# Performance work log

Hardware: AMD Instinct MI355X
Metric: run time of the kernel (lower is better)

## Reference

```python
import jax, jax.numpy as jnp
import numpy as np

B, S, D, O = 16, 1024, 512, 512
THRESH = 0.9
NEG_SLOPE = 0.2  # PyG GATConv default leaky_relu slope


def setup_inputs() -> dict:
    key = jax.random.key(0)
    kx, kw, kas, kad, kb = jax.random.split(key, 5)
    # uniform in [0.2, 1) so cosine similarities straddle the 0.9 threshold
    x = jax.random.uniform(kx, (B, S, D), dtype=jnp.float32, minval=0.2, maxval=1.0)
    scale = 1.0 / np.sqrt(D)
    W = jax.random.normal(kw, (D, O), dtype=jnp.float32) * scale       # GATConv lin weight
    att_src = jax.random.normal(kas, (O,), dtype=jnp.float32) * scale  # att_src [1,1,O] squeezed
    att_dst = jax.random.normal(kad, (O,), dtype=jnp.float32) * scale  # att_dst [1,1,O] squeezed
    bias = jnp.zeros((O,), dtype=jnp.float32)
    return {"distilled_features": x, "W": W, "att_src": att_src, "att_dst": att_dst, "bias": bias}


def reference(distilled_features, W, att_src, att_dst, bias):
    x = distilled_features  # [B, S, D]
    s = x.shape[1]
    # --- edge construction: cosine similarity > 0.9, i < j, edge i->j (src->dst) ---
    norm = jnp.sqrt(jnp.sum(x * x, axis=-1, keepdims=True))
    normed = x / jnp.maximum(norm, 1e-12)  # F.normalize eps
    sim = jnp.einsum('bsd,btd->bst', normed, normed)  # [B, S, S], symmetric
    # adj[b, dst, src] = True if edge src->dst exists
    src_lt_dst = jnp.tril(jnp.ones((s, s), dtype=bool), k=-1)  # [dst, src] with src < dst
    eye = jnp.eye(s, dtype=bool)                                # self-loops (PyG default)
    adj = ((sim > THRESH) & src_lt_dst[None]) | eye[None]       # [B, dst, src]
    # --- GATConv, heads=1 (dropout inactive at inference) ---
    h = jnp.einsum('bsd,do->bso', x, W)            # [B, S, O]
    a_src = jnp.einsum('bso,o->bs', h, att_src)    # per-source logit
    a_dst = jnp.einsum('bso,o->bs', h, att_dst)    # per-dest logit
    e = jax.nn.leaky_relu(a_dst[:, :, None] + a_src[:, None, :], negative_slope=NEG_SLOPE)
    e = jnp.where(adj, e, -jnp.inf)
    attn = jax.nn.softmax(e, axis=-1)              # softmax over sources per dest
    out = jnp.einsum('bts,bso->bto', attn, h) + bias
    return jax.nn.relu(out)
```

## Files before the change

### kernel.cpp

```cpp
#include <hip/hip_runtime.h>
#include <hip/hip_bf16.h>
#include <stdint.h>

#define NB 16
#define NS 1024
#define ND 512
#define NO 512
#define NROW (NB*NS)
#define SIM_BAND 1.5e-3f
#define LIST_CAP 524288

typedef float f32x4 __attribute__((ext_vector_type(4)));
typedef _Float16 f16x8 __attribute__((ext_vector_type(8)));

__global__ __launch_bounds__(256) void k_prep_w2(const float* __restrict__ W,
                                                 const float* __restrict__ att_src,
                                                 const float* __restrict__ att_dst,
                                                 _Float16* __restrict__ Wf,
                                                 float* __restrict__ watt_s,
                                                 float* __restrict__ watt_d) {
  __shared__ float as_[512], ad_[512];
  int blk = blockIdx.x, tid = threadIdx.x;
  if (blk < 32) {
    int mt = blk>>3, k0c = blk&7;
    size_t base = ((size_t)(mt*8 + k0c))*8192;
    #pragma unroll
    for (int pp = 0; pp < 4; ++pp) {
      int id = pp*256 + tid;
      int kb = id>>9, m = (id>>6)&7, g = (id>>4)&3, r = id&15;
      int o = mt*128 + m*16 + r;
      int d0 = k0c*64 + kb*32 + g*8;
      union { _Float16 h[8]; uint4 u; } pk;
      #pragma unroll
      for (int j = 0; j < 8; ++j) pk.h[j] = (_Float16)W[(size_t)(d0+j)*NO + o];
      *(uint4*)&Wf[base + id*8] = pk.u;
    }
  } else {
    as_[tid] = att_src[tid]; as_[tid+256] = att_src[tid+256];
    ad_[tid] = att_dst[tid]; ad_[tid+256] = att_dst[tid+256];
    __syncthreads();
    int d = (blk-32)*256 + tid;
    const float* wr = W + (size_t)d*NO;
    float s = 0.f, dd = 0.f;
    for (int o = 0; o < NO; o += 4) {
      float4 w = *(const float4*)&wr[o];
      s  = fmaf(w.x, as_[o], fmaf(w.y, as_[o+1], fmaf(w.z, as_[o+2], fmaf(w.w, as_[o+3], s))));
      dd = fmaf(w.x, ad_[o], fmaf(w.y, ad_[o+1], fmaf(w.z, ad_[o+2], fmaf(w.w, ad_[o+3], dd))));
    }
    watt_s[d] = s;
    watt_d[d] = dd;
  }
}

__global__ __launch_bounds__(256) void k_prep_y(const float* __restrict__ x,
                                                _Float16* __restrict__ yf,
                                                float* __restrict__ rnorm,
                                                float* __restrict__ a_src,
                                                float* __restrict__ a_dst,
                                                const float* __restrict__ watt_s,
                                                const float* __restrict__ watt_d,
                                                int* __restrict__ counter) {
  __shared__ float ws_[512], wd_[512];
  int tid = threadIdx.x, blk = blockIdx.x;
  if (blk == 0 && tid == 0) *counter = 0;
  ws_[tid] = watt_s[tid]; ws_[tid+256] = watt_s[tid+256];
  wd_[tid] = watt_d[tid]; wd_[tid+256] = watt_d[tid+256];
  __syncthreads();
  int r = tid>>2, q = tid&3;
  int grow = blk*64 + r;
  const float* xr = x + (size_t)grow*ND + q*128;
  float ssq = 0.f, as = 0.f, ad = 0.f;
  #pragma unroll
  for (int c8 = 0; c8 < 16; ++c8) {
    float4 v0 = *(const float4*)&xr[c8*8];
    float4 v1 = *(const float4*)&xr[c8*8+4];
    float vv[8] = {v0.x,v0.y,v0.z,v0.w,v1.x,v1.y,v1.z,v1.w};
    #pragma unroll
    for (int j = 0; j < 8; ++j) {
      int c = q*128 + c8*8 + j;
      ssq = fmaf(vv[j], vv[j], ssq);
      as  = fmaf(vv[j], ws_[c], as);
      ad  = fmaf(vv[j], wd_[c], ad);
    }
  }
  ssq += __shfl_xor(ssq, 1, 64); ssq += __shfl_xor(ssq, 2, 64);
  as  += __shfl_xor(as, 1, 64);  as  += __shfl_xor(as, 2, 64);
  ad  += __shfl_xor(ad, 1, 64);  ad  += __shfl_xor(ad, 2, 64);
  float rn = 1.0f / fmaxf(sqrtf(ssq), 1e-12f);
  if (q == 0) { rnorm[grow] = rn; a_src[grow] = as; a_dst[grow] = ad; }
  int trow = grow & (NS-1), b = grow >> 10;
  int m = (trow>>4)&7, rr = trow&15;
  size_t tilebase = ((size_t)(b*8 + (trow>>7)))*65536;
  #pragma unroll
  for (int c8 = 0; c8 < 16; ++c8) {
    int col = q*128 + c8*8;
    int k0c = col>>6, cc = col&63, kb = cc>>5, g = (cc>>3)&3;
    int id = kb*512 + m*64 + g*16 + rr;
    size_t off = tilebase + (size_t)k0c*8192 + id*8;
    float4 v0 = *(const float4*)&xr[c8*8];
    float4 v1 = *(const float4*)&xr[c8*8+4];
    float vv[8] = {v0.x,v0.y,v0.z,v0.w,v1.x,v1.y,v1.z,v1.w};
    union { _Float16 h[8]; uint4 u; } pk;
    #pragma unroll
    for (int j = 0; j < 8; ++j) pk.h[j] = (_Float16)(vv[j]*rn);
    *(uint4*)&yf[off] = pk.u;
  }
}

#define FRAG_LD(AH, BH, APTR, BPTR, h) do { \
    _Pragma("unroll") \
    for (int q_ = 0; q_ < 4; ++q_) { \
      AH[q_] = *(const f16x8*)&APTR[Abase + (size_t)(h)*4096 + (size_t)(aq + q_)*512]; \
      BH[q_] = *(const f16x8*)&BPTR[Bbase + (size_t)(h)*4096 + (size_t)(bq + q_)*512]; \
    } \
  } while(0)

#define MFMA16(AH, BH) do { \
    _Pragma("unroll") \
    for (int mi_ = 0; mi_ < 4; ++mi_) \
      _Pragma("unroll") \
      for (int ni_ = 0; ni_ < 4; ++ni_) \
        acc[mi_][ni_] = __builtin_amdgcn_mfma_f32_16x16x32_f16(AH[mi_], BH[ni_], acc[mi_][ni_], 0,0,0); \
  } while(0)

__global__ __launch_bounds__(256) void k_sim_ht(const _Float16* __restrict__ yf,
                                                const _Float16* __restrict__ Wf,
                                                const float* __restrict__ rnorm,
                                                uint16_t* __restrict__ Mbits,
                                                unsigned int* __restrict__ list,
                                                int* __restrict__ counter,
                                                _Float16* __restrict__ htf) {
  __shared__ __align__(16) _Float16 sbuf[16384];
  int bid0 = blockIdx.x;
  int tid = threadIdx.x, wid = tid>>6, lane = tid&63;
  int wm = (wid>>1)*64, wn = (wid&1)*64;
  int aq = (wm>>4), bq = (wn>>4);
  if (bid0 < 576) {
    int swz = (bid0 & 7)*72 + (bid0 >> 3);
    int b = swz / 36, p = swz - b*36;
    int ti = 0;
    while ((ti+1)*(ti+2)/2 <= p) ++ti;
    int tj = p - ti*(ti+1)/2;
    size_t Abase = ((size_t)(b*8+ti))*65536 + (size_t)lane*8;
    size_t Bbase = ((size_t)(b*8+tj))*65536 + (size_t)lane*8;
    f32x4 acc[4][4] = {};
    f16x8 A0[4], B0[4], A1[4], B1[4];
    FRAG_LD(A0, B0, yf, yf, 0);
    for (int hp = 0; hp < 8; ++hp) {
      FRAG_LD(A1, B1, yf, yf, 2*hp+1);
      MFMA16(A0, B0);
      if (hp < 7) FRAG_LD(A0, B0, yf, yf, 2*hp+2);
      MFMA16(A1, B1);
    }
    int hi = lane>>4, colL = lane&15;
    #pragma unroll
    for (int mi = 0; mi < 4; ++mi) {
      #pragma unroll
      for (int r2 = 0; r2 < 4; ++r2) {
        int t_g = ti*128 + wm + mi*16 + hi*4 + r2;
        int git = b*NS + t_g;
        #pragma unroll
        for (int ni = 0; ni < 4; ++ni) {
          int s_g = tj*128 + wn + ni*16 + colL;
          float sim = acc[mi][ni][r2];
          bool bit = (s_g == t_g) || (s_g < t_g && sim > 0.9f);
          bool cond = (s_g < t_g) && (fabsf(sim - 0.9f) <= SIM_BAND);
          unsigned long long bb = __ballot(cond);
          if (bb) {
            int leader = __ffsll((unsigned long long)bb) - 1;
            int base = 0;
            if (lane == leader) base = atomicAdd(counter, __popcll(bb));
            base = __shfl(base, leader, 64);
            if (cond) {
              int idx = base + __popcll(bb & ((1ULL<<lane)-1ULL));
              if (idx < LIST_CAP) list[idx] = ((unsigned)b<<20) | ((unsigned)t_g<<10) | (unsigned)s_g;
            }
          }
          unsigned long long bal = __ballot(bit);
          if (colL == 0) {
            uint16_t slice = (uint16_t)((bal >> (hi*16)) & 0xFFFFull);
            Mbits[(size_t)git*64 + ((tj*128 + wn + ni*16)>>4)] = slice;
          }
        }
      }
    }
  } else {
    int bidh = bid0 - 576;
    int swz = (bidh&7)*64 + (bidh>>3);
    int mt = swz&3, it = swz>>2;
    int b = it>>3, tblk = it&7;
    size_t Abase = ((size_t)mt)*65536 + (size_t)lane*8;
    size_t Bbase = ((size_t)(b*8+tblk))*65536 + (size_t)lane*8;
    f32x4 acc[4][4] = {};
    f16x8 A0[4], B0[4], A1[4], B1[4];
    FRAG_LD(A0, B0, Wf, yf, 0);
    for (int hp = 0; hp < 8; ++hp) {
      FRAG_LD(A1, B1, Wf, yf, 2*hp+1);
      MFMA16(A0, B0);
      if (hp < 7) FRAG_LD(A0, B0, Wf, yf, 2*hp+2);
      MFMA16(A1, B1);
    }
    {
      int rbase = (lane>>4)*4, colL = lane&15;
      #pragma unroll
      for (int ni = 0; ni < 4; ++ni) {
        int i_local = wn + ni*16 + colL;
        int gn = it*128 + i_local;
        float xn = 1.0f / rnorm[gn];
        int tsel = i_local>>6, ic = i_local&63;
        int kb = ic>>5, g = (ic>>3)&3, j = ic&7;
        int base = tsel*8192 + (kb*512 + g*16)*8 + j;
        #pragma unroll
        for (int mi = 0; mi < 4; ++mi)
          #pragma unroll
          for (int r2 = 0; r2 < 4; ++r2) {
            int o_local = wm + mi*16 + rbase + r2;
            int m = o_local>>4, r = o_local&15;
            sbuf[base + (m*64 + r)*8] = (_Float16)(acc[mi][ni][r2] * xn);
          }
      }
    }
    __syncthreads();
    {
      size_t gbase = ((size_t)((mt*NB + b)*16 + tblk*2))*8192;
      const uint4* src = (const uint4*)sbuf;
      uint4* dst = (uint4*)(htf + gbase);
      #pragma unroll
      for (int k = 0; k < 8; ++k) dst[tid + k*256] = src[tid + k*256];
    }
  }
}

__global__ __launch_bounds__(256) void k_recheck(const float* __restrict__ x,
                                                 const float* __restrict__ rnorm,
                                                 uint32_t* __restrict__ Mw,
                                                 const unsigned int* __restrict__ list,
                                                 const int* __restrict__ counter) {
  int n = *counter;
  if (n > LIST_CAP) n = LIST_CAP;
  int lane = threadIdx.x & 63;
  int gwave = blockIdx.x*4 + (threadIdx.x>>6);
  for (int p = gwave; p < n; p += 8192) {
    unsigned v = list[p];
    int b = v>>20, t = (v>>10)&1023, s = v&1023;
    const float* xt = x + ((size_t)(b*NS + t))*ND + lane*8;
    const float* xs = x + ((size_t)(b*NS + s))*ND + lane*8;
    float4 t0 = *(const float4*)xt;
    float4 t1 = *(const float4*)(xt+4);
    float4 s0 = *(const float4*)xs;
    float4 s1 = *(const float4*)(xs+4);
    float d = 0.f;
    d = fmaf(t0.x,s0.x, fmaf(t0.y,s0.y, fmaf(t0.z,s0.z, fmaf(t0.w,s0.w, d))));
    d = fmaf(t1.x,s1.x, fmaf(t1.y,s1.y, fmaf(t1.z,s1.z, fmaf(t1.w,s1.w, d))));
    #pragma unroll
    for (int off = 32; off > 0; off >>= 1) d += __shfl_xor(d, off, 64);
    if (lane == 0) {
      float sim = d * rnorm[b*NS+t] * rnorm[b*NS+s];
      int git = b*NS + t;
      uint32_t bmask = 1u << (s&31);
      if (sim > 0.9f) atomicOr (&Mw[(size_t)git*32 + (s>>5)], bmask);
      else            atomicAnd(&Mw[(size_t)git*32 + (s>>5)], ~bmask);
    }
  }
}

__global__ __launch_bounds__(256) void k_softmax(const uint32_t* __restrict__ Mw,
                                                 const float* __restrict__ a_src,
                                                 const float* __restrict__ a_dst,
                                                 _Float16* __restrict__ Pf) {
  __shared__ __align__(16) _Float16 pbuf[4][1032];
  int wid = threadIdx.x>>6, lane = threadIdx.x&63;
  int rowid = blockIdx.x*4 + wid;
  int t = rowid & (NS-1), b = rowid >> 10;
  int n = t + 1;
  const float* as = a_src + b*NS;
  float adv = a_dst[rowid];
  uint32_t w = Mw[(size_t)rowid*32 + (lane>>1)];
  uint32_t bits16 = (lane&1) ? (w>>16) : (w & 0xFFFFu);
  int s0 = lane*16;
  float4 a0 = *(const float4*)&as[s0];
  float4 a1 = *(const float4*)&as[s0+4];
  float4 a2 = *(const float4*)&as[s0+8];
  float4 a3 = *(const float4*)&as[s0+12];
  float va[16] = {a0.x,a0.y,a0.z,a0.w, a1.x,a1.y,a1.z,a1.w,
                  a2.x,a2.y,a2.z,a2.w, a3.x,a3.y,a3.z,a3.w};
  float pr[16];
  float lm = -INFINITY;
  #pragma unroll
  for (int k = 0; k < 16; ++k) {
    int s = s0 + k;
    bool on = (s < n) && ((bits16>>k)&1);
    float vv = adv + va[k];
    float v = (vv > 0.f) ? vv : 0.2f*vv;
    pr[k] = on ? v : -INFINITY;
    lm = fmaxf(lm, pr[k]);
  }
  #pragma unroll
  for (int off = 32; off > 0; off >>= 1) lm = fmaxf(lm, __shfl_xor(lm, off, 64));
  float ls = 0.f;
  #pragma unroll
  for (int k = 0; k < 16; ++k) { pr[k] = __expf(pr[k] - lm); ls += pr[k]; }
  #pragma unroll
  for (int off = 32; off > 0; off >>= 1) ls += __shfl_xor(ls, off, 64);
  float inv = 1.0f / ls;
  union { _Float16 hh[8]; uint4 u; } pk0, pk1;
  #pragma unroll
  for (int j = 0; j < 8; ++j) pk0.hh[j] = (_Float16)(pr[j]*inv);
  #pragma unroll
  for (int j = 0; j < 8; ++j) pk1.hh[j] = (_Float16)(pr[8+j]*inv);
  *(uint4*)&pbuf[wid][s0]   = pk0.u;
  *(uint4*)&pbuf[wid][s0+8] = pk1.u;
  __syncthreads();
  int t0 = (blockIdx.x*4) & (NS-1);
  int b0 = (blockIdx.x*4) >> 10;
  int end = ((t0 >> 7) + 1) << 7;
  int m = (t0>>4)&7, r0 = t0&15;
  size_t tbase = ((size_t)(b0*8 + (t0>>7)))*131072;
  int nslots = (end>>3)*4;
  for (int u = threadIdx.x; u < nslots; u += 256) {
    int rr = u&3, c8 = u>>2;
    int icol = c8*8;
    int k0c = icol>>6, kb = (icol>>5)&1, g = (icol>>3)&3;
    uint4 v = *(const uint4*)&pbuf[rr][icol];
    *(uint4*)&Pf[tbase + (size_t)k0c*8192 + (size_t)(kb*512 + m*64 + g*16 + r0 + rr)*8] = v;
  }
}

__global__ __launch_bounds__(256) void k_pv(const _Float16* __restrict__ Pf,
                                            const _Float16* __restrict__ htf,
                                            const float* __restrict__ bias,
                                            float* __restrict__ out) {
  int bid = blockIdx.x;
  int swz = (bid&7)*64 + (bid>>3);
  int b = swz>>5, rem = swz&31, mt = rem>>2, nt = rem&3;
  int tid = threadIdx.x, wid = tid>>6, lane = tid&63;
  int wm = (wid>>1)*64, wn = (wid&1)*64;
  size_t Abase = ((size_t)((b*8 + mt)*16))*8192 + (size_t)lane*8;
  size_t Bbase = ((size_t)((nt*NB + b)*16))*8192 + (size_t)lane*8;
  int aq = (wm>>4), bq = (wn>>4);
  f32x4 acc[4][4] = {};
  int nhp = 2*(mt+1);
  f16x8 A0[4], B0[4], A1[4], B1[4];
  FRAG_LD(A0, B0, Pf, htf, 0);
  for (int hp = 0; hp < nhp; ++hp) {
    FRAG_LD(A1, B1, Pf, htf, 2*hp+1);
    MFMA16(A0, B0);
    if (hp < nhp-1) FRAG_LD(A0, B0, Pf, htf, 2*hp+2);
    MFMA16(A1, B1);
  }
  int m0 = mt*128, n0 = nt*128;
  int rbase = (lane>>4)*4, col = lane&15;
  #pragma unroll
  for (int mi = 0; mi < 4; ++mi)
    #pragma unroll
    for (int ni = 0; ni < 4; ++ni) {
      int gm = m0 + wm + mi*16 + rbase;
      int gn = n0 + wn + ni*16 + col;
      float bv = bias[gn];
      #pragma unroll
      for (int r2 = 0; r2 < 4; ++r2)
        out[((size_t)b*NS + gm + r2)*NO + gn] = fmaxf(acc[mi][ni][r2] + bv, 0.0f);
    }
}

extern "C" void kernel_launch(void* const* d_in, const int* in_sizes, int n_in,
                              void* d_out, int out_size, void* d_ws, size_t ws_size,
                              hipStream_t stream) {
  (void)in_sizes; (void)n_in; (void)out_size; (void)ws_size;
  const float* x       = (const float*)d_in[0];
  const float* W       = (const float*)d_in[1];
  const float* att_src = (const float*)d_in[2];
  const float* att_dst = (const float*)d_in[3];
  const float* bias    = (const float*)d_in[4];
  float* out = (float*)d_out;

  char* ws = (char*)d_ws;
  _Float16*     yf    = (_Float16*)    (ws + 0);
  _Float16*     htf   = (_Float16*)    (ws + 16777216);
  _Float16*     Pf    = (_Float16*)    (ws + 33554432);
  uint16_t*     Mbits = (uint16_t*)    (ws + 67108864);
  _Float16*     Wf    = (_Float16*)    (ws + 69206016);
  float*        watt_s= (float*)       (ws + 69730304);
  float*        watt_d= (float*)       (ws + 69732352);
  float*        rnorm = (float*)       (ws + 69734400);
  float*        a_src = (float*)       (ws + 69799936);
  float*        a_dst = (float*)       (ws + 69865472);
  unsigned int* list  = (unsigned int*)(ws + 69931008);
  int*          cnt   = (int*)         (ws + 72028160);

  k_prep_w2<<<dim3(34),   dim3(256), 0, stream>>>(W, att_src, att_dst, Wf, watt_s, watt_d);
  k_prep_y <<<dim3(256),  dim3(256), 0, stream>>>(x, yf, rnorm, a_src, a_dst, watt_s, watt_d, cnt);
  k_sim_ht <<<dim3(1088), dim3(256), 0, stream>>>(yf, Wf, rnorm, Mbits, list, cnt, htf);
  k_recheck<<<dim3(2048), dim3(256), 0, stream>>>(x, rnorm, (uint32_t*)Mbits, list, cnt);
  k_softmax<<<dim3(4096), dim3(256), 0, stream>>>((const uint32_t*)Mbits, a_src, a_dst, Pf);
  k_pv     <<<dim3(512),  dim3(256), 0, stream>>>(Pf, htf, bias, out);
}
```

Before: 107.6 us.

## Fold borderline-similarity recheck into softmax via a per-edge band bitmask

```diff
diff --git a/kernel.cpp b/kernel.cpp
--- a/kernel.cpp
+++ b/kernel.cpp
@@ -8,7 +8,6 @@
 #define NO 512
 #define NROW (NB*NS)
 #define SIM_BAND 1.5e-3f
-#define LIST_CAP 524288
 
 typedef float f32x4 __attribute__((ext_vector_type(4)));
 typedef _Float16 f16x8 __attribute__((ext_vector_type(8)));
@@ -58,11 +57,9 @@
                                                 float* __restrict__ a_src,
                                                 float* __restrict__ a_dst,
                                                 const float* __restrict__ watt_s,
-                                                const float* __restrict__ watt_d,
-                                                int* __restrict__ counter) {
+                                                const float* __restrict__ watt_d) {
   __shared__ float ws_[512], wd_[512];
   int tid = threadIdx.x, blk = blockIdx.x;
-  if (blk == 0 && tid == 0) *counter = 0;
   ws_[tid] = watt_s[tid]; ws_[tid+256] = watt_s[tid+256];
   wd_[tid] = watt_d[tid]; wd_[tid+256] = watt_d[tid+256];
   __syncthreads();
@@ -127,8 +124,7 @@
                                                 const _Float16* __restrict__ Wf,
                                                 const float* __restrict__ rnorm,
                                                 uint16_t* __restrict__ Mbits,
-                                                unsigned int* __restrict__ list,
-                                                int* __restrict__ counter,
+                                                uint16_t* __restrict__ Bbits,
                                                 _Float16* __restrict__ htf) {
   __shared__ __align__(16) _Float16 sbuf[16384];
   int bid0 = blockIdx.x;
@@ -163,23 +159,14 @@
         for (int ni = 0; ni < 4; ++ni) {
           int s_g = tj*128 + wn + ni*16 + colL;
           float sim = acc[mi][ni][r2];
-          bool bit = (s_g == t_g) || (s_g < t_g && sim > 0.9f);
+          bool bit  = (s_g == t_g) || (s_g < t_g && sim > 0.9f);
           bool cond = (s_g < t_g) && (fabsf(sim - 0.9f) <= SIM_BAND);
-          unsigned long long bb = __ballot(cond);
-          if (bb) {
-            int leader = __ffsll((unsigned long long)bb) - 1;
-            int base = 0;
-            if (lane == leader) base = atomicAdd(counter, __popcll(bb));
-            base = __shfl(base, leader, 64);
-            if (cond) {
-              int idx = base + __popcll(bb & ((1ULL<<lane)-1ULL));
-              if (idx < LIST_CAP) list[idx] = ((unsigned)b<<20) | ((unsigned)t_g<<10) | (unsigned)s_g;
-            }
-          }
           unsigned long long bal = __ballot(bit);
+          unsigned long long bb  = __ballot(cond);
           if (colL == 0) {
-            uint16_t slice = (uint16_t)((bal >> (hi*16)) & 0xFFFFull);
-            Mbits[(size_t)git*64 + ((tj*128 + wn + ni*16)>>4)] = slice;
+            int widx = (tj*128 + wn + ni*16)>>4;
+            Mbits[(size_t)git*64 + widx] = (uint16_t)((bal >> (hi*16)) & 0xFFFFull);
+            Bbits[(size_t)git*64 + widx] = (uint16_t)((bb  >> (hi*16)) & 0xFFFFull);
           }
         }
       }
@@ -231,40 +218,10 @@
   }
 }
 
-__global__ __launch_bounds__(256) void k_recheck(const float* __restrict__ x,
+__global__ __launch_bounds__(256) void k_softmax(const uint32_t* __restrict__ Mw,
+                                                 const uint32_t* __restrict__ Bw,
+                                                 const float* __restrict__ x,
                                                  const float* __restrict__ rnorm,
-                                                 uint32_t* __restrict__ Mw,
-                                                 const unsigned int* __restrict__ list,
-                                                 const int* __restrict__ counter) {
-  int n = *counter;
-  if (n > LIST_CAP) n = LIST_CAP;
-  int lane = threadIdx.x & 63;
-  int gwave = blockIdx.x*4 + (threadIdx.x>>6);
-  for (int p = gwave; p < n; p += 8192) {
-    unsigned v = list[p];
-    int b = v>>20, t = (v>>10)&1023, s = v&1023;
-    const float* xt = x + ((size_t)(b*NS + t))*ND + lane*8;
-    const float* xs = x + ((size_t)(b*NS + s))*ND + lane*8;
-    float4 t0 = *(const float4*)xt;
-    float4 t1 = *(const float4*)(xt+4);
-    float4 s0 = *(const float4*)xs;
-    float4 s1 = *(const float4*)(xs+4);
-    float d = 0.f;
-    d = fmaf(t0.x,s0.x, fmaf(t0.y,s0.y, fmaf(t0.z,s0.z, fmaf(t0.w,s0.w, d))));
-    d = fmaf(t1.x,s1.x, fmaf(t1.y,s1.y, fmaf(t1.z,s1.z, fmaf(t1.w,s1.w, d))));
-    #pragma unroll
-    for (int off = 32; off > 0; off >>= 1) d += __shfl_xor(d, off, 64);
-    if (lane == 0) {
-      float sim = d * rnorm[b*NS+t] * rnorm[b*NS+s];
-      int git = b*NS + t;
-      uint32_t bmask = 1u << (s&31);
-      if (sim > 0.9f) atomicOr (&Mw[(size_t)git*32 + (s>>5)], bmask);
-      else            atomicAnd(&Mw[(size_t)git*32 + (s>>5)], ~bmask);
-    }
-  }
-}
-
-__global__ __launch_bounds__(256) void k_softmax(const uint32_t* __restrict__ Mw,
                                                  const float* __restrict__ a_src,
                                                  const float* __restrict__ a_dst,
                                                  _Float16* __restrict__ Pf) {
@@ -277,7 +234,14 @@
   float adv = a_dst[rowid];
   uint32_t w = Mw[(size_t)rowid*32 + (lane>>1)];
   uint32_t bits16 = (lane&1) ? (w>>16) : (w & 0xFFFFu);
+  uint32_t w2 = Bw[(size_t)rowid*32 + (lane>>1)];
+  uint32_t bb16 = (lane&1) ? (w2>>16) : (w2 & 0xFFFFu);
   int s0 = lane*16;
+  {
+    int rem = n - s0;
+    uint32_t gmask = (rem <= 0) ? 0u : (rem >= 16 ? 0xFFFFu : ((1u<<rem)-1u));
+    bb16 &= gmask;
+  }
   float4 a0 = *(const float4*)&as[s0];
   float4 a1 = *(const float4*)&as[s0+4];
   float4 a2 = *(const float4*)&as[s0+8];
@@ -285,7 +249,6 @@
   float va[16] = {a0.x,a0.y,a0.z,a0.w, a1.x,a1.y,a1.z,a1.w,
                   a2.x,a2.y,a2.z,a2.w, a3.x,a3.y,a3.z,a3.w};
   float pr[16];
-  float lm = -INFINITY;
   #pragma unroll
   for (int k = 0; k < 16; ++k) {
     int s = s0 + k;
@@ -293,8 +256,49 @@
     float vv = adv + va[k];
     float v = (vv > 0.f) ? vv : 0.2f*vv;
     pr[k] = on ? v : -INFINITY;
-    lm = fmaxf(lm, pr[k]);
-  }
+  }
+  uint32_t fix_on = 0u, fix_off = 0u;
+  unsigned long long anyb = __ballot(bb16 != 0u);
+  if (anyb) {
+    float rnt = rnorm[rowid];
+    const float* xt = x + (size_t)rowid*ND + lane*8;
+    float4 t0v = *(const float4*)xt;
+    float4 t1v = *(const float4*)(xt+4);
+    while (anyb) {
+      int src_lane = __ffsll(anyb) - 1;
+      anyb &= anyb - 1ULL;
+      unsigned bits = __shfl(bb16, src_lane, 64);
+      while (bits) {
+        int k = __ffs(bits) - 1;
+        bits &= bits - 1u;
+        int s = src_lane*16 + k;
+        const float* xs = x + ((size_t)(b*NS + s))*ND + lane*8;
+        float4 s0v = *(const float4*)xs;
+        float4 s1v = *(const float4*)(xs+4);
+        float d = 0.f;
+        d = fmaf(t0v.x,s0v.x, fmaf(t0v.y,s0v.y, fmaf(t0v.z,s0v.z, fmaf(t0v.w,s0v.w, d))));
+        d = fmaf(t1v.x,s1v.x, fmaf(t1v.y,s1v.y, fmaf(t1v.z,s1v.z, fmaf(t1v.w,s1v.w, d))));
+        #pragma unroll
+        for (int off = 32; off > 0; off >>= 1) d += __shfl_xor(d, off, 64);
+        float sim = d * rnt * rnorm[b*NS+s];
+        bool on2 = sim > 0.9f;
+        if (lane == src_lane) {
+          if (on2) fix_on  |= (1u<<k);
+          else     fix_off |= (1u<<k);
+        }
+      }
+    }
+  }
+  #pragma unroll
+  for (int k = 0; k < 16; ++k) {
+    float vv = adv + va[k];
+    float v = (vv > 0.f) ? vv : 0.2f*vv;
+    if ((fix_on >>k)&1) pr[k] = v;
+    if ((fix_off>>k)&1) pr[k] = -INFINITY;
+  }
+  float lm = -INFINITY;
+  #pragma unroll
+  for (int k = 0; k < 16; ++k) lm = fmaxf(lm, pr[k]);
   #pragma unroll
   for (int off = 32; off > 0; off >>= 1) lm = fmaxf(lm, __shfl_xor(lm, off, 64));
   float ls = 0.f;
@@ -379,19 +383,18 @@
   _Float16*     htf   = (_Float16*)    (ws + 16777216);
   _Float16*     Pf    = (_Float16*)    (ws + 33554432);
   uint16_t*     Mbits = (uint16_t*)    (ws + 67108864);
-  _Float16*     Wf    = (_Float16*)    (ws + 69206016);
-  float*        watt_s= (float*)       (ws + 69730304);
-  float*        watt_d= (float*)       (ws + 69732352);
-  float*        rnorm = (float*)       (ws + 69734400);
-  float*        a_src = (float*)       (ws + 69799936);
-  float*        a_dst = (float*)       (ws + 69865472);
-  unsigned int* list  = (unsigned int*)(ws + 69931008);
-  int*          cnt   = (int*)         (ws + 72028160);
+  uint16_t*     Bbits = (uint16_t*)    (ws + 69206016);
+  _Float16*     Wf    = (_Float16*)    (ws + 71303168);
+  float*        watt_s= (float*)       (ws + 71827456);
+  float*        watt_d= (float*)       (ws + 71829504);
+  float*        rnorm = (float*)       (ws + 71831552);
+  float*        a_src = (float*)       (ws + 71897088);
+  float*        a_dst = (float*)       (ws + 71962624);
 
   k_prep_w2<<<dim3(34),   dim3(256), 0, stream>>>(W, att_src, att_dst, Wf, watt_s, watt_d);
-  k_prep_y <<<dim3(256),  dim3(256), 0, stream>>>(x, yf, rnorm, a_src, a_dst, watt_s, watt_d, cnt);
-  k_sim_ht <<<dim3(1088), dim3(256), 0, stream>>>(yf, Wf, rnorm, Mbits, list, cnt, htf);
-  k_recheck<<<dim3(2048), dim3(256), 0, stream>>>(x, rnorm, (uint32_t*)Mbits, list, cnt);
-  k_softmax<<<dim3(4096), dim3(256), 0, stream>>>((const uint32_t*)Mbits, a_src, a_dst, Pf);
+  k_prep_y <<<dim3(256),  dim3(256), 0, stream>>>(x, yf, rnorm, a_src, a_dst, watt_s, watt_d);
+  k_sim_ht <<<dim3(1088), dim3(256), 0, stream>>>(yf, Wf, rnorm, Mbits, Bbits, htf);
+  k_softmax<<<dim3(4096), dim3(256), 0, stream>>>((const uint32_t*)Mbits, (const uint32_t*)Bbits,
+                                                  x, rnorm, a_src, a_dst, Pf);
   k_pv     <<<dim3(512),  dim3(256), 0, stream>>>(Pf, htf, bias, out);
 }
```

New measurement: 107.2 us. No clear change (-0.4%).
